# Kernel optimization log

Measured on AMD Instinct MI355X. Metric: run time of the kernel, lower is better.

## Reference

```python
import jax, jax.numpy as jnp
import numpy as np

N, E, G = 50000, 800000, 512
C = 128          # in_channels = hidden_out_channel = out_channel
K = 3            # Chebyshev order (nb_filters)
NUM_EMB = 119    # largest OGB atom feature cardinality (padded common table)
EPS = 1e-5


def setup_inputs() -> dict:
    key = jax.random.key(0)
    ks = jax.random.split(key, 12)
    s = 0.05
    return {
        "atom_emb": jax.random.normal(ks[0], (9, NUM_EMB, C), jnp.float32) * s,
        "W1": jax.random.normal(ks[1], (K, C, C), jnp.float32) * s,
        "b1": jnp.zeros((C,), jnp.float32),
        "W3": jax.random.normal(ks[2], (K, C, C), jnp.float32) * s,
        "b3": jnp.zeros((C,), jnp.float32),
        "gamma": jnp.ones((C,), jnp.float32),
        "beta": jnp.zeros((C,), jnp.float32),
        "lw1": jax.random.normal(ks[3], (C, 16), jnp.float32) * s,
        "lb1": jnp.zeros((16,), jnp.float32),
        "lw2": jax.random.normal(ks[4], (16, 2), jnp.float32) * s,
        "lb2": jnp.zeros((2,), jnp.float32),
        "x": jax.random.randint(ks[5], (N, 9), 0, 2),
        "edge_index": jax.random.randint(ks[6], (2, E), 0, N),
        "batch": jnp.sort(jax.random.randint(ks[7], (N,), 0, G)),
    }


def _cheb_conv(h, row, col, norm, W, b):
    # PyG ChebConv, sym norm, lambda_max=2 => Lhat = -D^{-1/2} A D^{-1/2} (zero diag)
    def Lhat(z):
        return jax.ops.segment_sum(norm[:, None] * z[col], row, num_segments=N)
    Tx1 = Lhat(h)                      # T_1 = Lhat x
    Tx2 = 2.0 * Lhat(Tx1) - h          # T_2 = 2 Lhat T_1 - T_0
    return h @ W[0] + Tx1 @ W[1] + Tx2 @ W[2] + b


def reference(atom_emb, W1, b1, W3, b3, gamma, beta, lw1, lb1, lw2, lb2,
              x, edge_index, batch):
    row, col = edge_index[0], edge_index[1]
    # symmetric normalization weights (deg computed on row, as in get_laplacian)
    deg = jax.ops.segment_sum(jnp.ones((E,), jnp.float32), row, num_segments=N)
    dis = jnp.where(deg > 0, jax.lax.rsqrt(jnp.maximum(deg, 1.0)), 0.0)
    norm = -(dis[row] * dis[col])      # [E]

    # AtomEncoder: sum of 9 per-feature embeddings -> [N, C]
    h = atom_emb[jnp.arange(9), x].sum(axis=1)

    h = jax.nn.relu(_cheb_conv(h, row, col, norm, W1, b1))   # conv1
    h = jax.nn.relu(_cheb_conv(h, row, col, norm, W3, b3))   # conv3 (conv2 unused)

    # BatchNorm over nodes (training-mode batch stats, biased var)
    mu = h.mean(axis=0)
    var = jnp.mean((h - mu) ** 2, axis=0)
    h = (h - mu) * jax.lax.rsqrt(var + EPS) * gamma + beta

    # global_mean_pool over graphs
    sums = jax.ops.segment_sum(h, batch, num_segments=G)
    cnt = jax.ops.segment_sum(jnp.ones((N,), jnp.float32), batch, num_segments=G)
    pooled = sums / jnp.maximum(cnt, 1.0)[:, None]           # [G, C]

    out = jax.nn.relu(pooled @ lw1 + lb1) @ lw2 + lb2        # [G, 2]
    return out
```

## Files before the change

kernel.cpp:

```cpp
#include <hip/hip_runtime.h>
#include <hip/hip_bf16.h>

typedef __hip_bfloat16 bf16;
#define BN_EPS 1e-5f

typedef __attribute__((ext_vector_type(8))) short bf16x8;
typedef __attribute__((ext_vector_type(4))) float f32x4;

__device__ __forceinline__ float b2f(bf16 v){ return __bfloat162float(v); }
__device__ __forceinline__ float bu2f(unsigned short u){
  union { unsigned int i; float f; } x; x.i = ((unsigned int)u) << 16; return x.f;
}
__device__ __forceinline__ unsigned short f2bu(float f){
  bf16 b = __float2bfloat16(f);
  union { bf16 b; unsigned short u; } x; x.b = b; return x.u;
}
__device__ __forceinline__ float ldw(const void* p, size_t i, int wf){
  return wf ? ((const float*)p)[i] : b2f(((const bf16*)p)[i]);
}
__device__ __forceinline__ void up2(unsigned int w, float& lo, float& hi){
  union { unsigned int i; float f; } L, H;
  L.i = w << 16; H.i = w & 0xffff0000u;
  lo = L.f; hi = H.f;
}

__global__ void k_zero(int* __restrict__ p, int n,
                       const unsigned int* __restrict__ gbits, int* __restrict__ flag){
  int i = blockIdx.x * blockDim.x + threadIdx.x;
  if (i == 0) *flag = (gbits[0] == 0x3F800000u) ? 1 : 0;
  if (i < n) p[i] = 0;
}

__global__ __launch_bounds__(256) void k_bhist(const int* __restrict__ row, int E,
                                               int* __restrict__ gcnt){
  __shared__ int hist[256];
  int t = threadIdx.x;
  hist[t] = 0;
  __syncthreads();
  int base = blockIdx.x * 4096;
  #pragma unroll
  for (int j = 0; j < 16; ++j){
    int e = base + (j << 8) + t;
    if (e < E) atomicAdd(&hist[row[e] >> 8], 1);
  }
  __syncthreads();
  int h = hist[t];
  if (h > 0) atomicAdd(&gcnt[t], h);
}

__global__ __launch_bounds__(256) void k_bbase(const int* __restrict__ gcnt,
    int* __restrict__ bucketBase, int* __restrict__ gcur, int* __restrict__ rp, int N){
  __shared__ int ss[256];
  int t = threadIdx.x;
  int v = gcnt[t];
  ss[t] = v; __syncthreads();
  for (int o = 1; o < 256; o <<= 1){
    int u = (t >= o) ? ss[t - o] : 0;
    __syncthreads();
    ss[t] += u;
    __syncthreads();
  }
  int ex = ss[t] - v;
  bucketBase[t] = ex;
  gcur[t] = ex;
  if (t == 255){ bucketBase[256] = ss[255]; rp[N] = ss[255]; }
}

__global__ __launch_bounds__(256) void k_prep(int N,
    const void* __restrict__ Wa, unsigned short* __restrict__ WTa,
    const void* __restrict__ Wb, unsigned short* __restrict__ WTb,
    const void* __restrict__ emb, const int* __restrict__ x, int NE,
    unsigned short* __restrict__ h, const int* __restrict__ flag){
  int b = blockIdx.x;
  int t = threadIdx.x;
  int wf = *flag;
  if (b < 384){
    int id = b * 256 + t;
    const void* W = (id < 49152) ? Wa : Wb;
    unsigned short* WT = (id < 49152) ? WTa : WTb;
    int i = (id < 49152) ? id : id - 49152;
    int r = i >> 7, n = i & 127;
    WT[(size_t)n * 384 + r] = f2bu(ldw(W, (size_t)r * 128 + n, wf));
    return;
  }
  int gid = (b - 384) * 256 + t;
  int n = gid >> 4, c8 = (gid & 15) << 3;
  if (n >= N) return;
  float s[8];
  #pragma unroll
  for (int j = 0; j < 8; ++j) s[j] = 0.f;
  #pragma unroll
  for (int f = 0; f < 9; ++f){
    int idx = x[n * 9 + f];
    size_t base = ((size_t)(f * NE + idx) << 7) + c8;
    if (wf){
      const float* ep = (const float*)emb + base;
      #pragma unroll
      for (int j = 0; j < 8; ++j) s[j] += ep[j];
    } else {
      uint4 v = *(const uint4*)((const unsigned short*)emb + base);
      float lo, hi;
      up2(v.x, lo, hi); s[0] += lo; s[1] += hi;
      up2(v.y, lo, hi); s[2] += lo; s[3] += hi;
      up2(v.z, lo, hi); s[4] += lo; s[5] += hi;
      up2(v.w, lo, hi); s[6] += lo; s[7] += hi;
    }
  }
  uint4 r;
  r.x = ((unsigned int)f2bu(s[1]) << 16) | f2bu(s[0]);
  r.y = ((unsigned int)f2bu(s[3]) << 16) | f2bu(s[2]);
  r.z = ((unsigned int)f2bu(s[5]) << 16) | f2bu(s[4]);
  r.w = ((unsigned int)f2bu(s[7]) << 16) | f2bu(s[6]);
  *(uint4*)(h + ((size_t)n << 7) + c8) = r;
}

__global__ __launch_bounds__(256) void k_bfill1(const int* __restrict__ row,
    const int* __restrict__ col, int E,
    int* __restrict__ gcur, unsigned int* __restrict__ ebuf){
  __shared__ int hist[256];
  __shared__ int curs[256];
  int t = threadIdx.x;
  hist[t] = 0;
  __syncthreads();
  int base = blockIdx.x * 4096;
  int r[16], c[16];
  #pragma unroll
  for (int j = 0; j < 16; ++j){
    int e = base + (j << 8) + t;
    if (e < E){
      r[j] = row[e]; c[j] = col[e];
      atomicAdd(&hist[r[j] >> 8], 1);
    } else r[j] = -1;
  }
  __syncthreads();
  int h = hist[t];
  if (h > 0) curs[t] = atomicAdd(&gcur[t], h);
  __syncthreads();
  #pragma unroll
  for (int j = 0; j < 16; ++j){
    if (r[j] >= 0){
      int p = atomicAdd(&curs[r[j] >> 8], 1);
      ebuf[p] = ((unsigned int)c[j] << 8) | ((unsigned int)r[j] & 255u);
    }
  }
}

__global__ __launch_bounds__(256) void k_bfill2a(const unsigned int* __restrict__ ebuf,
    const int* __restrict__ bucketBase, int N,
    int* __restrict__ rp, float* __restrict__ dis){
  __shared__ int cnt[256];
  __shared__ int ss[256];
  int b = blockIdx.x, t = threadIdx.x;
  cnt[t] = 0;
  __syncthreads();
  int beg = bucketBase[b], end = bucketBase[b + 1];
  for (int p = beg + t; p < end; p += 256)
    atomicAdd(&cnt[ebuf[p] & 255u], 1);
  __syncthreads();
  int v = cnt[t];
  ss[t] = v; __syncthreads();
  for (int o = 1; o < 256; o <<= 1){
    int u = (t >= o) ? ss[t - o] : 0;
    __syncthreads();
    ss[t] += u;
    __syncthreads();
  }
  int idx = (b << 8) + t;
  if (idx < N){
    rp[idx] = beg + ss[t] - v;
    dis[idx] = (v > 0) ? rsqrtf((float)v) : 0.f;
  }
}

__global__ __launch_bounds__(256) void k_bfill2b(const unsigned int* __restrict__ ebuf,
    const int* __restrict__ bucketBase, const int* __restrict__ rp, int N,
    const float* __restrict__ dis, int2* __restrict__ cpack){
  __shared__ int lcur[256];
  __shared__ float sdis[256];
  int b = blockIdx.x, t = threadIdx.x;
  int idx = (b << 8) + t;
  lcur[t] = (idx < N) ? rp[idx] : 0;
  sdis[t] = (idx < N) ? dis[idx] : 0.f;
  __syncthreads();
  int beg = bucketBase[b], end = bucketBase[b + 1];
  for (int p = beg + t; p < end; p += 256){
    unsigned int pw = ebuf[p];
    int c = (int)(pw >> 8);
    int rl = (int)(pw & 255u);
    float nm = -(sdis[rl] * dis[c]);
    int slot = atomicAdd(&lcur[rl], 1);
    cpack[slot] = make_int2(c, __float_as_int(nm));
  }
}

__global__ __launch_bounds__(256) void k_spmm(const unsigned short* __restrict__ in,
    const int* __restrict__ rp, const int2* __restrict__ cpack,
    float alpha, const unsigned short* __restrict__ other, float beta,
    unsigned short* __restrict__ out, int N){
  int w = (blockIdx.x * 256 + threadIdx.x) >> 6;
  int lane = threadIdx.x & 63;
  if (w >= N) return;
  int half = lane >> 5, hl = lane & 31;
  int p0 = rp[w], p1 = rp[w + 1];
  float a0 = 0.f, a1 = 0.f, a2 = 0.f, a3 = 0.f;
  for (int p = p0; p < p1; p += 64){
    int m = p1 - p; if (m > 64) m = 64;
    int cj = 0; float nj = 0.f;
    if (lane < m){
      int2 pk = cpack[p + lane];
      cj = pk.x; nj = __int_as_float(pk.y);
    }
    for (int j = 0; j < m; j += 4){
      int e0 = j + half, e1 = j + 2 + half;
      int c0 = (e0 < m) ? __shfl(cj, e0) : -1;
      float w0 = __shfl(nj, e0);
      int c1 = (e1 < m) ? __shfl(cj, e1) : -1;
      float w1 = __shfl(nj, e1);
      if (c0 >= 0){
        ushort4 v = *(const ushort4*)(in + (((size_t)c0) << 7) + (hl << 2));
        a0 += w0 * bu2f(v.x); a1 += w0 * bu2f(v.y);
        a2 += w0 * bu2f(v.z); a3 += w0 * bu2f(v.w);
      }
      if (c1 >= 0){
        ushort4 v = *(const ushort4*)(in + (((size_t)c1) << 7) + (hl << 2));
        a0 += w1 * bu2f(v.x); a1 += w1 * bu2f(v.y);
        a2 += w1 * bu2f(v.z); a3 += w1 * bu2f(v.w);
      }
    }
  }
  a0 += __shfl_xor(a0, 32);
  a1 += __shfl_xor(a1, 32);
  a2 += __shfl_xor(a2, 32);
  a3 += __shfl_xor(a3, 32);
  if (half == 0){
    size_t o = (((size_t)w) << 7) + (hl << 2);
    a0 *= alpha; a1 *= alpha; a2 *= alpha; a3 *= alpha;
    if (other){
      ushort4 ov = *(const ushort4*)(other + o);
      a0 += beta * bu2f(ov.x); a1 += beta * bu2f(ov.y);
      a2 += beta * bu2f(ov.z); a3 += beta * bu2f(ov.w);
    }
    ushort4 r;
    r.x = f2bu(a0); r.y = f2bu(a1); r.z = f2bu(a2); r.w = f2bu(a3);
    *(ushort4*)(out + o) = r;
  }
}

__global__ __launch_bounds__(256) void k_conv(const unsigned short* __restrict__ X,
    const unsigned short* __restrict__ T1, const unsigned short* __restrict__ T2,
    const unsigned short* __restrict__ WT,
    const void* __restrict__ bias,
    unsigned short* __restrict__ Y, int N, const int* __restrict__ flag,
    float* __restrict__ bns){
  int wf = *flag;
  __shared__ unsigned short As[128 * 40];
  __shared__ unsigned short Ws[128 * 40];
  int t = threadIdx.x;
  int wv = t >> 6, lane = t & 63;
  int m16 = lane & 15, quad = lane >> 4;
  int n0 = blockIdx.x * 128;

  f32x4 acc[2][8];
  #pragma unroll
  for (int i = 0; i < 2; ++i)
    #pragma unroll
    for (int j = 0; j < 8; ++j) acc[i][j] = (f32x4){0.f, 0.f, 0.f, 0.f};

  for (int kc = 0; kc < 12; ++kc){
    const unsigned short* src = (kc < 4) ? X : ((kc < 8) ? T1 : T2);
    int koff = (kc & 3) << 5;
    int kg = kc << 5;
    #pragma unroll
    for (int i = 0; i < 2; ++i){
      int id = t + (i << 8);
      int r = id >> 2, ks = id & 3;
      int node = n0 + r;
      uint4 v = make_uint4(0, 0, 0, 0);
      if (node < N) v = *(const uint4*)(src + ((size_t)node << 7) + koff + (ks << 3));
      *(uint4*)((void*)(As + r * 40 + (ks << 3))) = v;
    }
    #pragma unroll
    for (int i = 0; i < 2; ++i){
      int id = t + (i << 8);
      int n = id >> 2, ks = id & 3;
      uint4 v = *(const uint4*)(WT + (size_t)n * 384 + kg + (ks << 3));
      *(uint4*)((void*)(Ws + n * 40 + (ks << 3))) = v;
    }
    __syncthreads();
    bf16x8 af[2];
    af[0] = *(const bf16x8*)((const void*)(As + (32 * wv + m16) * 40 + (quad << 3)));
    af[1] = *(const bf16x8*)((const void*)(As + (32 * wv + 16 + m16) * 40 + (quad << 3)));
    #pragma unroll
    for (int tn = 0; tn < 8; ++tn){
      bf16x8 bf_ = *(const bf16x8*)((const void*)(Ws + (16 * tn + m16) * 40 + (quad << 3)));
      acc[0][tn] = __builtin_amdgcn_mfma_f32_16x16x32_bf16(af[0], bf_, acc[0][tn], 0, 0, 0);
      acc[1][tn] = __builtin_amdgcn_mfma_f32_16x16x32_bf16(af[1], bf_, acc[1][tn], 0, 0, 0);
    }
    __syncthreads();
  }
  float bv[8];
  #pragma unroll
  for (int tn = 0; tn < 8; ++tn) bv[tn] = ldw(bias, 16 * tn + m16, wf);
  float ps[8], pq[8];
  #pragma unroll
  for (int tn = 0; tn < 8; ++tn){ ps[tn] = 0.f; pq[tn] = 0.f; }
  #pragma unroll
  for (int ri = 0; ri < 2; ++ri){
    #pragma unroll
    for (int r = 0; r < 4; ++r){
      int node = n0 + 32 * wv + 16 * ri + quad * 4 + r;
      if (node < N){
        #pragma unroll
        for (int tn = 0; tn < 8; ++tn){
          float v = fmaxf(acc[ri][tn][r] + bv[tn], 0.f);
          Y[((size_t)node << 7) + 16 * tn + m16] = f2bu(v);
          ps[tn] += v; pq[tn] += v * v;
        }
      }
    }
  }
  if (bns){
    float* redf = (float*)As;
    int rg = (wv << 2) | quad;
    #pragma unroll
    for (int tn = 0; tn < 8; ++tn) redf[rg * 128 + tn * 16 + m16] = ps[tn];
    __syncthreads();
    if (t < 128){
      float a = 0.f;
      #pragma unroll
      for (int r = 0; r < 16; ++r) a += redf[r * 128 + t];
      atomicAdd(&bns[t], a);
    }
    __syncthreads();
    #pragma unroll
    for (int tn = 0; tn < 8; ++tn) redf[rg * 128 + tn * 16 + m16] = pq[tn];
    __syncthreads();
    if (t < 128){
      float a = 0.f;
      #pragma unroll
      for (int r = 0; r < 16; ++r) a += redf[r * 128 + t];
      atomicAdd(&bns[128 + t], a);
    }
  }
}

__device__ __forceinline__ int lbound(const int* a, int n, int key){
  int lo = 0, hi = n;
  while (lo < hi){ int mid = (lo + hi) >> 1; if (a[mid] < key) lo = mid + 1; else hi = mid; }
  return lo;
}

__global__ __launch_bounds__(128) void k_pool(const unsigned short* __restrict__ h,
    const int* __restrict__ batchv, int N, const float* __restrict__ bns,
    const void* __restrict__ gamma, const void* __restrict__ beta,
    const void* __restrict__ lw1, const void* __restrict__ lb1,
    const void* __restrict__ lw2, const void* __restrict__ lb2,
    void* __restrict__ out, const int* __restrict__ flag){
  int wf = *flag;
  int g = blockIdx.x;
  int t = threadIdx.x;
  int c8 = (t & 15) << 3;
  int rg = t >> 4;
  __shared__ int slo, shi;
  if (t == 0){ slo = lbound(batchv, N, g); shi = lbound(batchv, N, g + 1); }
  __syncthreads();
  int lo = slo, hi = shi, cnt = hi - lo;
  float s[8];
  #pragma unroll
  for (int j = 0; j < 8; ++j) s[j] = 0.f;
  for (int n = lo + rg; n < hi; n += 8){
    uint4 v = *(const uint4*)(h + ((size_t)n << 7) + c8);
    float a, b;
    up2(v.x, a, b); s[0] += a; s[1] += b;
    up2(v.y, a, b); s[2] += a; s[3] += b;
    up2(v.z, a, b); s[4] += a; s[5] += b;
    up2(v.w, a, b); s[6] += a; s[7] += b;
  }
  __shared__ float red[8][128];
  *(float4*)(&red[rg][c8])     = (float4){s[0], s[1], s[2], s[3]};
  *(float4*)(&red[rg][c8 + 4]) = (float4){s[4], s[5], s[6], s[7]};
  __syncthreads();
  int c = t;
  float acc = 0.f;
  #pragma unroll
  for (int r = 0; r < 8; ++r) acc += red[r][c];
  float pooled = acc / (float)(cnt > 0 ? cnt : 1);
  float mu = bns[c] / (float)N;
  float var = bns[128 + c] / (float)N - mu * mu;
  float sc = ldw(gamma, c, wf) * rsqrtf(var + BN_EPS);
  float sh = ldw(beta, c, wf) - mu * sc;
  float pb = (cnt > 0) ? (pooled * sc + sh) : 0.f;
  __shared__ float sp[128];
  __shared__ float hid[16];
  sp[c] = pb; __syncthreads();
  if (c < 16){
    float sm = ldw(lb1, c, wf);
    for (int i = 0; i < 128; ++i) sm += sp[i] * ldw(lw1, i * 16 + c, wf);
    hid[c] = fmaxf(sm, 0.f);
  }
  __syncthreads();
  if (c < 2){
    float sm = ldw(lb2, c, wf);
    for (int j = 0; j < 16; ++j) sm += hid[j] * ldw(lw2, j * 2 + c, wf);
    if (wf) ((float*)out)[g * 2 + c] = sm;
    else    ((bf16*)out)[g * 2 + c] = __float2bfloat16(sm);
  }
}

extern "C" void kernel_launch(void* const* d_in, const int* in_sizes, int n_in,
                              void* d_out, int out_size, void* d_ws, size_t ws_size,
                              hipStream_t stream){
  const void* emb   = d_in[0];
  const void* W1    = d_in[1];
  const void* b1    = d_in[2];
  const void* W3    = d_in[3];
  const void* b3    = d_in[4];
  const void* gamma = d_in[5];
  const void* beta  = d_in[6];
  const void* lw1   = d_in[7];
  const void* lb1   = d_in[8];
  const void* lw2   = d_in[9];
  const void* lb2   = d_in[10];
  const int* x      = (const int*)d_in[11];
  const int* ei     = (const int*)d_in[12];
  const int* batchv = (const int*)d_in[13];
  (void)n_in; (void)ws_size;

  int N  = in_sizes[13];
  int E  = in_sizes[12] / 2;
  int NE = in_sizes[0] / (9 * 128);
  int G  = out_size / 2;
  const int* row = ei;
  const int* col = ei + E;

  char* ws = (char*)d_ws;
  size_t off = 0;
  auto alloc = [&](size_t bytes) -> char* {
    char* p = ws + off;
    off += (bytes + 255) & ~(size_t)255;
    return p;
  };
  int*   flag = (int*)alloc(4);
  int*   gcnt = (int*)alloc(256 * 4);
  float* bns  = (float*)alloc(256 * 4);
  int*   bucketBase = (int*)alloc(257 * 4);
  int*   gcur = (int*)alloc(256 * 4);
  int*   rp   = (int*)alloc((size_t)(N + 1) * 4);
  float* dis  = (float*)alloc((size_t)N * 4);
  unsigned int* ebuf = (unsigned int*)alloc((size_t)E * 4);
  int2*  cpack = (int2*)alloc((size_t)E * 8);
  unsigned short* wt1 = (unsigned short*)alloc(49152 * 2);
  unsigned short* wt2 = (unsigned short*)alloc(49152 * 2);
  size_t fb = ((size_t)N * 128 * 2 + 255) & ~(size_t)255;
  unsigned short* Hf = (unsigned short*)alloc(fb);
  unsigned short* Tf = (unsigned short*)alloc(fb);
  unsigned short* Zf = (unsigned short*)alloc(fb);

  k_zero<<<2, 256, 0, stream>>>(gcnt, 512, (const unsigned int*)gamma, flag);

  int ebk = (E + 4095) / 4096;
  int NB  = (N + 255) / 256;
  k_bhist<<<ebk, 256, 0, stream>>>(row, E, gcnt);
  k_bbase<<<1, 256, 0, stream>>>(gcnt, bucketBase, gcur, rp, N);
  int pb = 384 + (int)(((size_t)N * 16 + 255) / 256);
  k_prep<<<pb, 256, 0, stream>>>(N, W1, wt1, W3, wt2, emb, x, NE, Hf, flag);
  k_bfill1<<<ebk, 256, 0, stream>>>(row, col, E, gcur, ebuf);
  k_bfill2a<<<NB, 256, 0, stream>>>(ebuf, bucketBase, N, rp, dis);
  k_bfill2b<<<NB, 256, 0, stream>>>(ebuf, bucketBase, rp, N, dis, cpack);

  int sb = (N + 3) / 4;
  int cb = (N + 127) / 128;
  k_spmm<<<sb, 256, 0, stream>>>(Hf, rp, cpack, 1.f, nullptr, 0.f, Tf, N);
  k_spmm<<<sb, 256, 0, stream>>>(Tf, rp, cpack, 2.f, Hf, -1.f, Zf, N);
  k_conv<<<cb, 256, 0, stream>>>(Hf, Tf, Zf, wt1, b1, Hf, N, flag, nullptr);
  k_spmm<<<sb, 256, 0, stream>>>(Hf, rp, cpack, 1.f, nullptr, 0.f, Tf, N);
  k_spmm<<<sb, 256, 0, stream>>>(Tf, rp, cpack, 2.f, Hf, -1.f, Zf, N);
  k_conv<<<cb, 256, 0, stream>>>(Hf, Tf, Zf, wt2, b3, Hf, N, flag, bns);

  k_pool<<<G, 128, 0, stream>>>(Hf, batchv, N, bns, gamma, beta, lw1, lb1, lw2, lb2,
                                d_out, flag);
}
```

Before: 353.5 us.

## Fuse graph preprocessing kernels into one cooperative kernel with grid syncs

The seven preprocessing launches (zero, bucket histogram, bucket base scan, prep, bucket fill, per-node scan, CSR pack) become one cooperative kernel that separates phases with grid.sync and uses grid-stride loops. The grid is sized from occupancy times CU count. The aim is to remove per-launch overhead and gaps between these small kernels. In exchange it adds grid-wide barrier cost, host-side property queries on every call, and lower parallelism inside phases that previously launched more blocks. Weight prep and embedding now run in the same phase as the bucket fill.

Result: slower. 851.1 us (+140.8%).

```diff
diff --git a/kernel.cpp b/kernel.cpp
--- a/kernel.cpp
+++ b/kernel.cpp
@@ -1,5 +1,8 @@
 #include <hip/hip_runtime.h>
+#include <hip/hip_cooperative_groups.h>
 #include <hip/hip_bf16.h>
+
+namespace cg = cooperative_groups;
 
 typedef __hip_bfloat16 bf16;
 #define BN_EPS 1e-5f
@@ -24,172 +27,174 @@
   lo = L.f; hi = H.f;
 }
 
-__global__ void k_zero(int* __restrict__ p, int n,
-                       const unsigned int* __restrict__ gbits, int* __restrict__ flag){
-  int i = blockIdx.x * blockDim.x + threadIdx.x;
-  if (i == 0) *flag = (gbits[0] == 0x3F800000u) ? 1 : 0;
-  if (i < n) p[i] = 0;
-}
-
-__global__ __launch_bounds__(256) void k_bhist(const int* __restrict__ row, int E,
-                                               int* __restrict__ gcnt){
-  __shared__ int hist[256];
-  int t = threadIdx.x;
-  hist[t] = 0;
-  __syncthreads();
-  int base = blockIdx.x * 4096;
-  #pragma unroll
-  for (int j = 0; j < 16; ++j){
-    int e = base + (j << 8) + t;
-    if (e < E) atomicAdd(&hist[row[e] >> 8], 1);
-  }
-  __syncthreads();
-  int h = hist[t];
-  if (h > 0) atomicAdd(&gcnt[t], h);
-}
-
-__global__ __launch_bounds__(256) void k_bbase(const int* __restrict__ gcnt,
-    int* __restrict__ bucketBase, int* __restrict__ gcur, int* __restrict__ rp, int N){
-  __shared__ int ss[256];
-  int t = threadIdx.x;
-  int v = gcnt[t];
-  ss[t] = v; __syncthreads();
-  for (int o = 1; o < 256; o <<= 1){
-    int u = (t >= o) ? ss[t - o] : 0;
-    __syncthreads();
-    ss[t] += u;
-    __syncthreads();
-  }
-  int ex = ss[t] - v;
-  bucketBase[t] = ex;
-  gcur[t] = ex;
-  if (t == 255){ bucketBase[256] = ss[255]; rp[N] = ss[255]; }
-}
-
-__global__ __launch_bounds__(256) void k_prep(int N,
+__global__ __launch_bounds__(256, 4) void k_graph(
+    const int* __restrict__ row, const int* __restrict__ col, int E, int N, int NE,
+    const unsigned int* __restrict__ gbits, int* __restrict__ flag,
+    int* __restrict__ gcnt, float* __restrict__ bns,
+    int* __restrict__ bucketBase, int* __restrict__ gcur,
+    int* __restrict__ rp, float* __restrict__ dis,
+    unsigned int* __restrict__ ebuf, int2* __restrict__ cpack,
     const void* __restrict__ Wa, unsigned short* __restrict__ WTa,
     const void* __restrict__ Wb, unsigned short* __restrict__ WTb,
-    const void* __restrict__ emb, const int* __restrict__ x, int NE,
-    unsigned short* __restrict__ h, const int* __restrict__ flag){
-  int b = blockIdx.x;
-  int t = threadIdx.x;
+    const void* __restrict__ emb, const int* __restrict__ x,
+    unsigned short* __restrict__ h)
+{
+  cg::grid_group grid = cg::this_grid();
+  __shared__ int sa[256];
+  __shared__ int sb[256];
+  __shared__ float sf[256];
+  int t = threadIdx.x, bid = blockIdx.x, GB = gridDim.x;
+  int nChunks = (E + 4095) >> 12;
+  int NB = (N + 255) >> 8;
+
+  if (bid == 0){
+    gcnt[t] = 0;
+    bns[t] = 0.f;
+    if (t == 0) *flag = (gbits[0] == 0x3F800000u) ? 1 : 0;
+  }
+  grid.sync();
+
+  for (int ch = bid; ch < nChunks; ch += GB){
+    sa[t] = 0;
+    __syncthreads();
+    int base = ch << 12;
+    #pragma unroll
+    for (int j = 0; j < 16; ++j){
+      int e = base + (j << 8) + t;
+      if (e < E) atomicAdd(&sa[row[e] >> 8], 1);
+    }
+    __syncthreads();
+    if (sa[t] > 0) atomicAdd(&gcnt[t], sa[t]);
+    __syncthreads();
+  }
+  grid.sync();
+
+  if (bid == 0){
+    int v = gcnt[t];
+    sa[t] = v; __syncthreads();
+    for (int o = 1; o < 256; o <<= 1){
+      int u = (t >= o) ? sa[t - o] : 0;
+      __syncthreads();
+      sa[t] += u;
+      __syncthreads();
+    }
+    int ex = sa[t] - v;
+    bucketBase[t] = ex;
+    gcur[t] = ex;
+    if (t == 255){ bucketBase[256] = sa[255]; rp[N] = sa[255]; }
+  }
+  grid.sync();
+
   int wf = *flag;
-  if (b < 384){
-    int id = b * 256 + t;
-    const void* W = (id < 49152) ? Wa : Wb;
-    unsigned short* WT = (id < 49152) ? WTa : WTb;
-    int i = (id < 49152) ? id : id - 49152;
-    int r = i >> 7, n = i & 127;
-    WT[(size_t)n * 384 + r] = f2bu(ldw(W, (size_t)r * 128 + n, wf));
-    return;
-  }
-  int gid = (b - 384) * 256 + t;
-  int n = gid >> 4, c8 = (gid & 15) << 3;
-  if (n >= N) return;
-  float s[8];
-  #pragma unroll
-  for (int j = 0; j < 8; ++j) s[j] = 0.f;
-  #pragma unroll
-  for (int f = 0; f < 9; ++f){
-    int idx = x[n * 9 + f];
-    size_t base = ((size_t)(f * NE + idx) << 7) + c8;
-    if (wf){
-      const float* ep = (const float*)emb + base;
-      #pragma unroll
-      for (int j = 0; j < 8; ++j) s[j] += ep[j];
+  int prepBlocks = 384 + (int)(((size_t)N * 16 + 255) >> 8);
+  for (int b = bid; b < prepBlocks; b += GB){
+    if (b < 384){
+      int id = b * 256 + t;
+      const void* W = (id < 49152) ? Wa : Wb;
+      unsigned short* WT = (id < 49152) ? WTa : WTb;
+      int i = (id < 49152) ? id : id - 49152;
+      int r = i >> 7, n = i & 127;
+      WT[(size_t)n * 384 + r] = f2bu(ldw(W, (size_t)r * 128 + n, wf));
     } else {
-      uint4 v = *(const uint4*)((const unsigned short*)emb + base);
-      float lo, hi;
-      up2(v.x, lo, hi); s[0] += lo; s[1] += hi;
-      up2(v.y, lo, hi); s[2] += lo; s[3] += hi;
-      up2(v.z, lo, hi); s[4] += lo; s[5] += hi;
-      up2(v.w, lo, hi); s[6] += lo; s[7] += hi;
-    }
-  }
-  uint4 r;
-  r.x = ((unsigned int)f2bu(s[1]) << 16) | f2bu(s[0]);
-  r.y = ((unsigned int)f2bu(s[3]) << 16) | f2bu(s[2]);
-  r.z = ((unsigned int)f2bu(s[5]) << 16) | f2bu(s[4]);
-  r.w = ((unsigned int)f2bu(s[7]) << 16) | f2bu(s[6]);
-  *(uint4*)(h + ((size_t)n << 7) + c8) = r;
-}
-
-__global__ __launch_bounds__(256) void k_bfill1(const int* __restrict__ row,
-    const int* __restrict__ col, int E,
-    int* __restrict__ gcur, unsigned int* __restrict__ ebuf){
-  __shared__ int hist[256];
-  __shared__ int curs[256];
-  int t = threadIdx.x;
-  hist[t] = 0;
-  __syncthreads();
-  int base = blockIdx.x * 4096;
-  int r[16], c[16];
-  #pragma unroll
-  for (int j = 0; j < 16; ++j){
-    int e = base + (j << 8) + t;
-    if (e < E){
-      r[j] = row[e]; c[j] = col[e];
-      atomicAdd(&hist[r[j] >> 8], 1);
-    } else r[j] = -1;
-  }
-  __syncthreads();
-  int h = hist[t];
-  if (h > 0) curs[t] = atomicAdd(&gcur[t], h);
-  __syncthreads();
-  #pragma unroll
-  for (int j = 0; j < 16; ++j){
-    if (r[j] >= 0){
-      int p = atomicAdd(&curs[r[j] >> 8], 1);
-      ebuf[p] = ((unsigned int)c[j] << 8) | ((unsigned int)r[j] & 255u);
-    }
-  }
-}
-
-__global__ __launch_bounds__(256) void k_bfill2a(const unsigned int* __restrict__ ebuf,
-    const int* __restrict__ bucketBase, int N,
-    int* __restrict__ rp, float* __restrict__ dis){
-  __shared__ int cnt[256];
-  __shared__ int ss[256];
-  int b = blockIdx.x, t = threadIdx.x;
-  cnt[t] = 0;
-  __syncthreads();
-  int beg = bucketBase[b], end = bucketBase[b + 1];
-  for (int p = beg + t; p < end; p += 256)
-    atomicAdd(&cnt[ebuf[p] & 255u], 1);
-  __syncthreads();
-  int v = cnt[t];
-  ss[t] = v; __syncthreads();
-  for (int o = 1; o < 256; o <<= 1){
-    int u = (t >= o) ? ss[t - o] : 0;
-    __syncthreads();
-    ss[t] += u;
-    __syncthreads();
-  }
-  int idx = (b << 8) + t;
-  if (idx < N){
-    rp[idx] = beg + ss[t] - v;
-    dis[idx] = (v > 0) ? rsqrtf((float)v) : 0.f;
-  }
-}
-
-__global__ __launch_bounds__(256) void k_bfill2b(const unsigned int* __restrict__ ebuf,
-    const int* __restrict__ bucketBase, const int* __restrict__ rp, int N,
-    const float* __restrict__ dis, int2* __restrict__ cpack){
-  __shared__ int lcur[256];
-  __shared__ float sdis[256];
-  int b = blockIdx.x, t = threadIdx.x;
-  int idx = (b << 8) + t;
-  lcur[t] = (idx < N) ? rp[idx] : 0;
-  sdis[t] = (idx < N) ? dis[idx] : 0.f;
-  __syncthreads();
-  int beg = bucketBase[b], end = bucketBase[b + 1];
-  for (int p = beg + t; p < end; p += 256){
-    unsigned int pw = ebuf[p];
-    int c = (int)(pw >> 8);
-    int rl = (int)(pw & 255u);
-    float nm = -(sdis[rl] * dis[c]);
-    int slot = atomicAdd(&lcur[rl], 1);
-    cpack[slot] = make_int2(c, __float_as_int(nm));
+      int gid = (b - 384) * 256 + t;
+      int n = gid >> 4, c8 = (gid & 15) << 3;
+      if (n < N){
+        float s[8];
+        #pragma unroll
+        for (int j = 0; j < 8; ++j) s[j] = 0.f;
+        #pragma unroll
+        for (int f = 0; f < 9; ++f){
+          int idx = x[n * 9 + f];
+          size_t base = ((size_t)(f * NE + idx) << 7) + c8;
+          if (wf){
+            const float* ep = (const float*)emb + base;
+            #pragma unroll
+            for (int j = 0; j < 8; ++j) s[j] += ep[j];
+          } else {
+            uint4 v = *(const uint4*)((const unsigned short*)emb + base);
+            float lo, hi;
+            up2(v.x, lo, hi); s[0] += lo; s[1] += hi;
+            up2(v.y, lo, hi); s[2] += lo; s[3] += hi;
+            up2(v.z, lo, hi); s[4] += lo; s[5] += hi;
+            up2(v.w, lo, hi); s[6] += lo; s[7] += hi;
+          }
+        }
+        uint4 r;
+        r.x = ((unsigned int)f2bu(s[1]) << 16) | f2bu(s[0]);
+        r.y = ((unsigned int)f2bu(s[3]) << 16) | f2bu(s[2]);
+        r.z = ((unsigned int)f2bu(s[5]) << 16) | f2bu(s[4]);
+        r.w = ((unsigned int)f2bu(s[7]) << 16) | f2bu(s[6]);
+        *(uint4*)(h + ((size_t)n << 7) + c8) = r;
+      }
+    }
+  }
+  for (int ch = bid; ch < nChunks; ch += GB){
+    sa[t] = 0;
+    __syncthreads();
+    int base = ch << 12;
+    int r[16], c[16];
+    #pragma unroll
+    for (int j = 0; j < 16; ++j){
+      int e = base + (j << 8) + t;
+      if (e < E){
+        r[j] = row[e]; c[j] = col[e];
+        atomicAdd(&sa[r[j] >> 8], 1);
+      } else r[j] = -1;
+    }
+    __syncthreads();
+    int hh = sa[t];
+    if (hh > 0) sb[t] = atomicAdd(&gcur[t], hh);
+    __syncthreads();
+    #pragma unroll
+    for (int j = 0; j < 16; ++j){
+      if (r[j] >= 0){
+        int p = atomicAdd(&sb[r[j] >> 8], 1);
+        ebuf[p] = ((unsigned int)c[j] << 8) | ((unsigned int)r[j] & 255u);
+      }
+    }
+    __syncthreads();
+  }
+  grid.sync();
+
+  for (int b = bid; b < NB; b += GB){
+    sa[t] = 0;
+    __syncthreads();
+    int beg = bucketBase[b], end = bucketBase[b + 1];
+    for (int p = beg + t; p < end; p += 256)
+      atomicAdd(&sa[ebuf[p] & 255u], 1);
+    __syncthreads();
+    int v = sa[t];
+    sb[t] = v; __syncthreads();
+    for (int o = 1; o < 256; o <<= 1){
+      int u = (t >= o) ? sb[t - o] : 0;
+      __syncthreads();
+      sb[t] += u;
+      __syncthreads();
+    }
+    int idx = (b << 8) + t;
+    if (idx < N){
+      rp[idx] = beg + sb[t] - v;
+      dis[idx] = (v > 0) ? rsqrtf((float)v) : 0.f;
+    }
+    __syncthreads();
+  }
+  grid.sync();
+
+  for (int b = bid; b < NB; b += GB){
+    int idx = (b << 8) + t;
+    sa[t] = (idx < N) ? rp[idx] : 0;
+    sf[t] = (idx < N) ? dis[idx] : 0.f;
+    __syncthreads();
+    int beg = bucketBase[b], end = bucketBase[b + 1];
+    for (int p = beg + t; p < end; p += 256){
+      unsigned int pw = ebuf[p];
+      int c = (int)(pw >> 8);
+      int rl = (int)(pw & 255u);
+      float nm = -(sf[rl] * dis[c]);
+      int slot = atomicAdd(&sa[rl], 1);
+      cpack[slot] = make_int2(c, __float_as_int(nm));
+    }
+    __syncthreads();
   }
 }
 
@@ -456,17 +461,32 @@
   unsigned short* Tf = (unsigned short*)alloc(fb);
   unsigned short* Zf = (unsigned short*)alloc(fb);
 
-  k_zero<<<2, 256, 0, stream>>>(gcnt, 512, (const unsigned int*)gamma, flag);
-
-  int ebk = (E + 4095) / 4096;
-  int NB  = (N + 255) / 256;
-  k_bhist<<<ebk, 256, 0, stream>>>(row, E, gcnt);
-  k_bbase<<<1, 256, 0, stream>>>(gcnt, bucketBase, gcur, rp, N);
-  int pb = 384 + (int)(((size_t)N * 16 + 255) / 256);
-  k_prep<<<pb, 256, 0, stream>>>(N, W1, wt1, W3, wt2, emb, x, NE, Hf, flag);
-  k_bfill1<<<ebk, 256, 0, stream>>>(row, col, E, gcur, ebuf);
-  k_bfill2a<<<NB, 256, 0, stream>>>(ebuf, bucketBase, N, rp, dis);
-  k_bfill2b<<<NB, 256, 0, stream>>>(ebuf, bucketBase, rp, N, dis, cpack);
+  int bpc = 0;
+  hipError_t oe = hipOccupancyMaxActiveBlocksPerMultiprocessor(&bpc, (const void*)k_graph, 256, 0);
+  if (oe != hipSuccess || bpc < 1) bpc = 2;
+  int nCU = 0;
+  {
+    hipDeviceProp_t props;
+    int dev = 0;
+    if (hipGetDevice(&dev) == hipSuccess &&
+        hipGetDeviceProperties(&props, dev) == hipSuccess)
+      nCU = props.multiProcessorCount;
+  }
+  if (nCU <= 0) nCU = 256;
+  int gb = bpc * nCU;
+  if (gb > 2048) gb = 2048;
+  if (gb < 256) gb = 256;
+
+  const unsigned int* gbits = (const unsigned int*)gamma;
+  void* kargs[] = {
+    (void*)&row, (void*)&col, (void*)&E, (void*)&N, (void*)&NE,
+    (void*)&gbits, (void*)&flag,
+    (void*)&gcnt, (void*)&bns, (void*)&bucketBase, (void*)&gcur,
+    (void*)&rp, (void*)&dis, (void*)&ebuf, (void*)&cpack,
+    (void*)&W1, (void*)&wt1, (void*)&W3, (void*)&wt2,
+    (void*)&emb, (void*)&x, (void*)&Hf
+  };
+  hipLaunchCooperativeKernel((void*)k_graph, dim3(gb), dim3(256), kargs, 0, stream);
 
   int sb = (N + 3) / 4;
   int cb = (N + 127) / 128;
```
